# Performance work log

Measured on AMD Instinct MI355X. Metric: run time of the kernel, lower is better.

## Reference

```python
import jax, jax.numpy as jnp
import numpy as np

DIM = 512
HID = 2048
EPS = 1e-5


def setup_inputs() -> dict:
    key = jax.random.key(0)
    ks = jax.random.split(key, 11)
    B, S = 256, 100
    def lin(kw, fan_in, fan_out):
        # torch Linear init: U(-1/sqrt(fan_in), 1/sqrt(fan_in)); stored as [in, out]
        bound = 1.0 / np.sqrt(fan_in)
        return jax.random.uniform(kw, (fan_in, fan_out), jnp.float32, -bound, bound)
    def bias(kb, fan_in, fan_out):
        bound = 1.0 / np.sqrt(fan_in)
        return jax.random.uniform(kb, (fan_out,), jnp.float32, -bound, bound)
    return {
        "x": jax.random.normal(ks[0], (B, S, DIM), jnp.float32),
        "W_w": lin(ks[1], DIM, HID),  "W_b": bias(ks[2], DIM, HID),
        "WK_w": lin(ks[3], HID, HID), "WK_b": bias(ks[4], HID, HID),
        "WQ_w": lin(ks[5], HID, HID), "WQ_b": bias(ks[6], HID, HID),
        "WV_w": lin(ks[7], HID, HID), "WV_b": bias(ks[8], HID, HID),
        "W2_w": lin(ks[9], HID, DIM), "W2_b": bias(ks[10], HID, DIM),
    }


def reference(x, W_w, W_b, WK_w, WK_b, WQ_w, WQ_b, WV_w, WV_b, W2_w, W2_b):
    S = x.shape[1]
    # torch: tril(ones, diagonal=1) -> token i may attend to j <= i+1
    mask = jnp.tril(jnp.ones((S, S), dtype=bool), k=1)
    residual = x
    h = jax.nn.relu(x @ W_w + W_b)            # [B,S,HID]
    K = h @ WK_w + WK_b
    Q = h @ WQ_w + WQ_b
    V = h @ WV_w + WV_b
    # note: original scales by sqrt(dim)=sqrt(512), not sqrt(hidden_dim)
    attn = jnp.einsum('bqh,bkh->bqk', Q, K) / np.sqrt(DIM)
    attn = jnp.where(mask, attn, -jnp.inf)
    attn = jax.nn.softmax(attn, axis=-1)
    o = jnp.einsum('bqk,bkh->bqh', attn, V)
    y = o @ W2_w + W2_b + residual            # [B,S,DIM]
    # F.layer_norm over x.shape[1:] == (S, DIM), no affine
    mu = jnp.mean(y, axis=(1, 2), keepdims=True)
    var = jnp.var(y, axis=(1, 2), keepdims=True)
    return (y - mu) * jax.lax.rsqrt(var + EPS)
```

## Files before the change

### kernel.cpp

```cpp
#include <hip/hip_runtime.h>
#include <hip/hip_bf16.h>

typedef unsigned int u32;
typedef unsigned short u16;
typedef __attribute__((ext_vector_type(4))) float f32x4;
typedef __attribute__((ext_vector_type(8))) short s16x8;
typedef __attribute__((ext_vector_type(4))) u16 u16x4;
typedef __attribute__((ext_vector_type(8))) u16 u16x8;

#define DEVFN __device__ __forceinline__

DEVFN u16 f2bf(float f) {
  u32 x = __builtin_bit_cast(u32, f);
  u32 r = x + 0x7fffu + ((x >> 16) & 1u);
  return (u16)(r >> 16);
}

DEVFN float bf2f(u16 b) { return __builtin_bit_cast(float, (u32)b << 16); }

DEVFN void gload_lds16(const u16* g, u16* l) {
  __builtin_amdgcn_global_load_lds((const __attribute__((address_space(1))) u32*)g,
                                   (__attribute__((address_space(3))) u32*)l, 16, 0, 0);
}

#define KQV_PHASE(Q, VMWAIT, DOSTAGE)                                          \
  {                                                                            \
    if (DOSTAGE) {                                                             \
      const int g_ = (Q) + 2;                                                  \
      const int sl_ = (g_ & 3) * 8192;                                         \
      const int k0_ = (g_ >> 1) * 64 + (g_ & 1) * 32;                          \
      gload_lds16(aS0 + k0_, smemw + sl_ + ldst);                              \
      gload_lds16(aS1 + k0_, smemw + sl_ + 4096 + ldst);                       \
      gload_lds16(bS0 + k0_, smemw + 32768 + sl_ + ldst);                      \
      gload_lds16(bS1 + k0_, smemw + 32768 + sl_ + 4096 + ldst);               \
    }                                                                          \
    VMWAIT;                                                                    \
    __builtin_amdgcn_s_barrier();                                              \
    {                                                                          \
      const int sl_ = (Q) & 3;                                                 \
      const u16* As_ = smem + sl_ * 8192;                                      \
      const u16* Bs_ = smem + 32768 + sl_ * 8192;                              \
      s16x8 fa_[8], fb_[4];                                                    \
      _Pragma("unroll") for (int mf = 0; mf < 8; ++mf)                         \
          fa_[mf] = *(const s16x8*)(As_ + baseA + mf * 512);                   \
      _Pragma("unroll") for (int nf = 0; nf < 4; ++nf)                         \
          fb_[nf] = *(const s16x8*)(Bs_ + baseB + nf * 512);                   \
      __builtin_amdgcn_s_setprio(1);                                           \
      _Pragma("unroll") for (int mf = 0; mf < 8; ++mf)                         \
        _Pragma("unroll") for (int nf = 0; nf < 4; ++nf)                       \
          acc[mf][nf] = __builtin_amdgcn_mfma_f32_16x16x32_bf16(               \
              fa_[mf], fb_[nf], acc[mf][nf], 0, 0, 0);                         \
      __builtin_amdgcn_s_setprio(0);                                           \
    }                                                                          \
    __builtin_amdgcn_sched_barrier(0);                                         \
  }

#define WAITV4 asm volatile("s_waitcnt vmcnt(4)" ::: "memory")
#define WAITV0 asm volatile("s_waitcnt vmcnt(0)" ::: "memory")
#define WAITNONE ((void)0)

template<int RELU>
__launch_bounds__(512, 2)
__global__ void gemm256(const u16* __restrict__ Ag, int lda,
                        const u16* __restrict__ Bg, int ldb,
                        u16* __restrict__ C, int ldc,
                        const float* __restrict__ bias,
                        int M, int K, int ntiles) {
  extern __shared__ u16 smem_dyn[];
  const u16* smem = smem_dyn;
  u16* smemw = smem_dyn;

  const int tid = threadIdx.x;
  const int lane = tid & 63, wave = tid >> 6;
  const int wm = wave >> 2, wn = wave & 3;
  const int l15 = lane & 15, l4 = lane >> 4;

  const int nwg = gridDim.x;
  const int q8 = nwg >> 3, r8 = nwg & 7;
  const int xcd = blockIdx.x & 7, io = blockIdx.x >> 3;
  const int wg = (xcd < r8) ? (xcd * (q8 + 1) + io)
                            : (r8 * (q8 + 1) + (xcd - r8) * q8 + io);
  const int m0 = (wg / ntiles) * 256, n0 = (wg % ntiles) * 256;

  const int chunkSwz = (l4 ^ ((l15 >> 1) & 3)) * 8;
  const int baseA = (wm * 128 + l15) * 32 + chunkSwz;
  const int baseB = (wn * 64 + l15) * 32 + chunkSwz;

  const int srow = tid >> 2;
  const int scol = (((tid & 3) ^ ((tid >> 3) & 3))) * 8;
  long ar0 = m0 + srow;        if (ar0 > M - 1) ar0 = M - 1;
  long ar1 = m0 + 128 + srow;  if (ar1 > M - 1) ar1 = M - 1;
  const u16* aS0 = Ag + ar0 * (long)lda + scol;
  const u16* aS1 = Ag + ar1 * (long)lda + scol;
  const u16* bS0 = Bg + (long)(n0 + srow) * ldb + scol;
  const u16* bS1 = Bg + (long)(n0 + 128 + srow) * ldb + scol;
  const int ldst = tid * 8;

  f32x4 acc[8][4];
#pragma unroll
  for (int i = 0; i < 8; ++i)
#pragma unroll
    for (int j = 0; j < 4; ++j) acc[i][j] = (f32x4){0.f, 0.f, 0.f, 0.f};

  const int NT = K >> 6;

  {
#pragma unroll
    for (int g_ = 0; g_ < 2; ++g_) {
      const int k0_ = g_ * 32;
      gload_lds16(aS0 + k0_, smemw + g_ * 8192 + ldst);
      gload_lds16(aS1 + k0_, smemw + g_ * 8192 + 4096 + ldst);
      gload_lds16(bS0 + k0_, smemw + 32768 + g_ * 8192 + ldst);
      gload_lds16(bS1 + k0_, smemw + 32768 + g_ * 8192 + 4096 + ldst);
    }
    __builtin_amdgcn_sched_barrier(0);
  }

  for (int t = 0; t < NT - 1; ++t) {
    KQV_PHASE(2 * t,     WAITV4, true);
    KQV_PHASE(2 * t + 1, WAITV4, true);
  }
  KQV_PHASE(2 * NT - 2, WAITV0,   false);
  KQV_PHASE(2 * NT - 1, WAITNONE, false);

#pragma unroll
  for (int mf = 0; mf < 8; ++mf) {
#pragma unroll
    for (int nf = 0; nf < 4; ++nf) {
      const int n = n0 + wn * 64 + nf * 16 + l15;
      const float bv = bias[n];
#pragma unroll
      for (int r = 0; r < 4; ++r) {
        const int s = wm * 128 + mf * 16 + l4 * 4 + r;
        if (m0 + s >= M) continue;
        float v = acc[mf][nf][r] + bv;
        if (RELU) v = v > 0.f ? v : 0.f;
        C[(long)(m0 + s) * ldc + n] = f2bf(v);
      }
    }
  }
}

template<int MODE>
__launch_bounds__(256)
__global__ void gemm_bt(const u16* __restrict__ Ag, int lda, int aRPB, int aRowMax,
                        const u16* __restrict__ Bg, int ldb, int bRPB, int bRowMax,
                        void* __restrict__ Cptr, int ldc, int cRPB, int cRowGuard,
                        const float* __restrict__ bias, const float* __restrict__ resid,
                        int K, float scale, float* __restrict__ part, int pbase,
                        long sliceE) {
  __shared__ __align__(16) u16 As[128 * 64];
  __shared__ __align__(16) u16 Bs[128 * 64];
  const int tid = threadIdx.x;
  const int lane = tid & 63, wid = tid >> 6;
  const int l15 = lane & 15, l4 = lane >> 4;
  const int wr = wid >> 1, wc = wid & 1;
  const int m0 = blockIdx.x * 128, n0 = blockIdx.y * 128;
  int b = blockIdx.z;
  int zslice = 0;
  long koff = 0;
  if (MODE == 6) { zslice = b & 3; koff = (long)zslice * K; b >>= 2; }

  const u16* aSrc[4];
  const u16* bSrc[4];
  u16* aDst[4];
  u16* bDst[4];
#pragma unroll
  for (int i = 0; i < 4; ++i) {
    int c = i * 256 + tid;
    int r = c >> 3, g = c & 7;
    long arow = (long)b * aRPB + m0 + r; if (arow > aRowMax) arow = aRowMax;
    aSrc[i] = Ag + arow * (long)lda + koff + g * 8;
    aDst[i] = &As[c * 8];
    long brow = (long)b * bRPB + n0 + r; if (brow > bRowMax) brow = bRowMax;
    bSrc[i] = Bg + brow * (long)ldb + koff + g * 8;
    bDst[i] = &Bs[c * 8];
  }

  f32x4 acc[4][4];
#pragma unroll
  for (int i = 0; i < 4; ++i)
#pragma unroll
    for (int j = 0; j < 4; ++j) acc[i][j] = (f32x4){0.f, 0.f, 0.f, 0.f};

  for (int kt = 0; kt < K; kt += 64) {
#pragma unroll
    for (int i = 0; i < 4; ++i) gload_lds16(aSrc[i] + kt, aDst[i]);
#pragma unroll
    for (int i = 0; i < 4; ++i) gload_lds16(bSrc[i] + kt, bDst[i]);
    __syncthreads();
#pragma unroll
    for (int kk = 0; kk < 2; ++kk) {
      s16x8 af[4], bfr[4];
#pragma unroll
      for (int mi = 0; mi < 4; ++mi) {
        int rr = wr * 64 + mi * 16 + l15;
        af[mi] = *(const s16x8*)&As[rr * 64 + kk * 32 + l4 * 8];
      }
#pragma unroll
      for (int ni = 0; ni < 4; ++ni) {
        int rr = wc * 64 + ni * 16 + l15;
        bfr[ni] = *(const s16x8*)&Bs[rr * 64 + kk * 32 + l4 * 8];
      }
#pragma unroll
      for (int mi = 0; mi < 4; ++mi)
#pragma unroll
        for (int ni = 0; ni < 4; ++ni)
          acc[mi][ni] = __builtin_amdgcn_mfma_f32_16x16x32_bf16(af[mi], bfr[ni], acc[mi][ni], 0, 0, 0);
    }
    __syncthreads();
  }

  const long cRow0 = (long)b * cRPB + m0;
  float lsum = 0.f, lsq = 0.f;
#pragma unroll
  for (int mi = 0; mi < 4; ++mi) {
#pragma unroll
    for (int ni = 0; ni < 4; ++ni) {
      const int n = n0 + wc * 64 + ni * 16 + l15;
      float bv = 0.f;
      if (MODE == 4) bv = bias[n];
#pragma unroll
      for (int r = 0; r < 4; ++r) {
        const int s = wr * 64 + mi * 16 + l4 * 4 + r;
        if (m0 + s < cRowGuard) {
          const long ci = (cRow0 + s) * (long)ldc + n;
          float v = acc[mi][ni][r];
          if (MODE == 3)      { ((u16*)Cptr)[ci] = f2bf(v); }
          else if (MODE == 6) { ((float*)Cptr)[(long)zslice * sliceE + ci] = v * scale; }
          else                { v += bv + resid[ci]; ((float*)Cptr)[ci] = v;
                                lsum += v; lsq += v * v; }
        }
      }
    }
  }

  if (MODE == 4) {
    float* shs = (float*)As;
    float* shq = (float*)Bs;
    shs[tid] = lsum; shq[tid] = lsq;
    __syncthreads();
    for (int off = 128; off; off >>= 1) {
      if (tid < off) { shs[tid] += shs[tid + off]; shq[tid] += shq[tid + off]; }
      __syncthreads();
    }
    if (tid == 0) {
      part[((long)pbase + b) * 8 + blockIdx.y * 2]     = shs[0];
      part[((long)pbase + b) * 8 + blockIdx.y * 2 + 1] = shq[0];
    }
  }
}

__launch_bounds__(256)
__global__ void softmax_rows(const float* __restrict__ S, u16* __restrict__ P,
                             long sliceE) {
  const int wid = threadIdx.x >> 6, lane = threadIdx.x & 63;
  const long rowg = (long)blockIdx.x * 4 + wid;
  const int i = (int)(rowg & 127);
  const float* srow = S + rowg * 128;
  u16* prow = P + rowg * 128;
  if (i >= 100) { prow[lane] = 0; prow[lane + 64] = 0; return; }
  const int jmax = (i + 1 < 99) ? i + 1 : 99;
  bool v0 = lane <= jmax, v1 = (lane + 64) <= jmax;
  float a0 = srow[lane]            + srow[sliceE + lane] +
             srow[2 * sliceE + lane] + srow[3 * sliceE + lane];
  float a1 = srow[lane + 64]            + srow[sliceE + lane + 64] +
             srow[2 * sliceE + lane + 64] + srow[3 * sliceE + lane + 64];
  float s0 = v0 ? a0 : -3e38f;
  float s1 = v1 ? a1 : -3e38f;
  float m = fmaxf(s0, s1);
#pragma unroll
  for (int off = 32; off; off >>= 1) m = fmaxf(m, __shfl_xor(m, off));
  float e0 = v0 ? __expf(s0 - m) : 0.f;
  float e1 = v1 ? __expf(s1 - m) : 0.f;
  float sum = e0 + e1;
#pragma unroll
  for (int off = 32; off; off >>= 1) sum += __shfl_xor(sum, off);
  float rs = 1.f / sum;
  prow[lane] = f2bf(e0 * rs);
  prow[lane + 64] = f2bf(e1 * rs);
}

__launch_bounds__(256)
__global__ void transpose_cast_w(const float* __restrict__ W, u16* __restrict__ Wt,
                                 int K, int N) {
  __shared__ __align__(16) float t[64][68];
  const int tid = threadIdx.x;
  const int n0 = blockIdx.x * 64, k0 = blockIdx.y * 64;
#pragma unroll
  for (int it = 0; it < 4; ++it) {
    int c = it * 256 + tid;
    int r = c >> 4, cc = (c & 15) * 4;
    f32x4 v = *(const f32x4*)&W[(long)(k0 + r) * N + n0 + cc];
    *(f32x4*)&t[r][cc] = v;
  }
  __syncthreads();
#pragma unroll
  for (int it = 0; it < 4; ++it) {
    int c = it * 256 + tid;
    int n = c >> 4, kk = (c & 15) * 4;
    u16x4 o;
#pragma unroll
    for (int j = 0; j < 4; ++j) o[j] = f2bf(t[kk + j][n]);
    *(u16x4*)&Wt[(long)(n0 + n) * K + k0 + kk] = o;
  }
}

__launch_bounds__(256)
__global__ void cast_f32_to_bf16(const float* __restrict__ in, u16* __restrict__ out, long n4) {
  for (long i = (long)blockIdx.x * 256 + threadIdx.x; i < n4; i += (long)gridDim.x * 256) {
    f32x4 v = *(const f32x4*)&in[i * 4];
    u16x4 o;
#pragma unroll
    for (int j = 0; j < 4; ++j) o[j] = f2bf(v[j]);
    *(u16x4*)&out[i * 4] = o;
  }
}

__launch_bounds__(256)
__global__ void rowdot_f32(const float* __restrict__ M, const float* __restrict__ v,
                           float* __restrict__ o, int ncols) {
  __shared__ float red[4];
  const float* r = M + (long)blockIdx.x * ncols;
  const int tid = threadIdx.x;
  float s = 0.f;
  for (int d = tid; d < ncols; d += 256) s += r[d] * v[d];
#pragma unroll
  for (int off = 32; off; off >>= 1) s += __shfl_down(s, off);
  if ((tid & 63) == 0) red[tid >> 6] = s;
  __syncthreads();
  if (tid == 0) o[blockIdx.x] = red[0] + red[1] + red[2] + red[3];
}

__launch_bounds__(256)
__global__ void bias_w2(const float* __restrict__ bV, const float* __restrict__ W2w,
                        float* __restrict__ o) {
  int n = blockIdx.x * 256 + threadIdx.x;
  float s = 0.f;
  for (int h = 0; h < 2048; ++h) s += bV[h] * W2w[h * 512 + n];
  o[n] = s;
}

__launch_bounds__(256)
__global__ void transpose_vt(const u16* __restrict__ V, u16* __restrict__ Vt,
                             int vstride, int nH) {
  __shared__ __align__(16) u16 t[64][72];
  const int tid = threadIdx.x;
  const int h0 = blockIdx.x * 64, s0 = blockIdx.y * 64, b = blockIdx.z;
#pragma unroll
  for (int it = 0; it < 2; ++it) {
    int c = it * 256 + tid;
    int s = c >> 3, hh = (c & 7) * 8;
    u16x8 v = {0, 0, 0, 0, 0, 0, 0, 0};
    if (s0 + s < 100) v = *(const u16x8*)&V[((long)b * 100 + s0 + s) * vstride + h0 + hh];
    *(u16x8*)&t[s][hh] = v;
  }
  __syncthreads();
#pragma unroll
  for (int it = 0; it < 2; ++it) {
    int c = it * 256 + tid;
    int h = c >> 3, ss = (c & 7) * 8;
    u16x8 o;
#pragma unroll
    for (int j = 0; j < 8; ++j) o[j] = t[ss + j][h];
    *(u16x8*)&Vt[((long)b * nH + h0 + h) * 128 + s0 + ss] = o;
  }
}

__launch_bounds__(256)
__global__ void ln_apply(float* __restrict__ y, const float* __restrict__ part) {
  const long i4 = (long)blockIdx.x * 256 + threadIdx.x;
  const int b = (int)(i4 / 12800);
  const float* pb = part + (long)b * 8;
  const float s = pb[0] + pb[2] + pb[4] + pb[6];
  const float q = pb[1] + pb[3] + pb[5] + pb[7];
  const float mean = s * (1.f / 51200.f);
  const float var = q * (1.f / 51200.f) - mean * mean;
  const float rstd = rsqrtf(var + 1e-5f);
  f32x4 v = *(const f32x4*)&y[i4 * 4];
#pragma unroll
  for (int j = 0; j < 4; ++j) v[j] = (v[j] - mean) * rstd;
  *(f32x4*)&y[i4 * 4] = v;
}

extern "C" void kernel_launch(void* const* d_in, const int* in_sizes, int n_in,
                              void* d_out, int out_size, void* d_ws, size_t ws_size,
                              hipStream_t stream) {
  const float* x    = (const float*)d_in[0];
  const float* W_w  = (const float*)d_in[1];
  const float* W_b  = (const float*)d_in[2];
  const float* WK_w = (const float*)d_in[3];
  const float* WK_b = (const float*)d_in[4];
  const float* WQ_w = (const float*)d_in[5];
  const float* WQ_b = (const float*)d_in[6];
  const float* WV_w = (const float*)d_in[7];
  const float* WV_b = (const float*)d_in[8];
  const float* W2_w = (const float*)d_in[9];
  const float* W2_b = (const float*)d_in[10];
  float* out = (float*)d_out;
  const float SC = 0.044194173824159216f;

  const size_t FIXED = 26214400ull + 2097152ull + 10485760ull + 2097152ull +
                       10240ull + 8192ull + 262144ull;
  const size_t PERB = 1347584ull;
  const size_t PREPOVL = 25165824ull + 65536ull;
  int CH = 256;
  if (ws_size == 0) CH = 32;
  else {
    while (CH > 4) {
      size_t chunkBytes = (size_t)CH * PERB;
      if (chunkBytes < PREPOVL) chunkBytes = PREPOVL;
      if (FIXED + chunkBytes + 4096 <= ws_size) break;
      CH >>= 1;
    }
  }
  const int NCH = 256 / CH;
  const int CHR = CH * 100;
  const int MT256 = (CHR + 255) / 256;
  const long SLICE = (long)CH * 16384;

  char* p = (char*)d_ws;
  auto carve = [&](size_t bytes) { char* r = p; p += (bytes + 255) & ~(size_t)255; return r; };
  u16* xb     = (u16*)carve(26214400);
  u16* W1t    = (u16*)carve(2097152);
  u16* WTt    = (u16*)carve(10485760);
  u16* W2t    = (u16*)carve(2097152);
  float* bias2 = (float*)carve(10240);
  float* part = (float*)carve(8192);
  char* chunk0 = p;
  u16* h    = (u16*)carve((size_t)CH * 409600);
  u16* TW   = (u16*)carve((size_t)CH * 512000);
  float* sc = (float*)carve((size_t)CH * 262144);
  u16* P    = (u16*)carve((size_t)CH * 32768);
  u16* VW2T = (u16*)carve((size_t)CH * 131072);
  u16* WVb = (u16*)chunk0;
  u16* WKb = WVb + 2048 * 2048;
  u16* WQb = WKb + 2048 * 2048;

  cast_f32_to_bf16<<<2048, 256, 0, stream>>>(x, xb, 3276800);
  cast_f32_to_bf16<<<1024, 256, 0, stream>>>(WV_w, WVb, 1048576);
  cast_f32_to_bf16<<<1024, 256, 0, stream>>>(WK_w, WKb, 1048576);
  cast_f32_to_bf16<<<1024, 256, 0, stream>>>(WQ_w, WQb, 1048576);
  transpose_cast_w<<<dim3(32, 8), 256, 0, stream>>>(W_w,  W1t, 512, 2048);
  transpose_cast_w<<<dim3(8, 32), 256, 0, stream>>>(W2_w, W2t, 2048, 512);
  gemm_bt<3><<<dim3(16, 16, 1), 256, 0, stream>>>(WKb, 2048, 0, 2047, WQb, 2048, 0, 2047,
                                                  WTt, 2048, 0, 1 << 30,
                                                  nullptr, nullptr, 2048, 1.f,
                                                  nullptr, 0, 0);
  gemm_bt<3><<<dim3(4, 16, 1), 256, 0, stream>>>(W2t, 2048, 0, 511, WVb, 2048, 0, 2047,
                                                 WTt + (size_t)2048 * 2048, 2048, 0, 1 << 30,
                                                 nullptr, nullptr, 2048, 1.f,
                                                 nullptr, 0, 0);
  rowdot_f32<<<2048, 256, 0, stream>>>(WK_w, WQ_b, bias2, 2048);
  bias_w2<<<2, 256, 0, stream>>>(WV_b, W2_w, bias2 + 2048);

  for (int c = 0; c < NCH; ++c) {
    const u16* xc = xb + (size_t)c * CHR * 512;
    const float* xf = x + (size_t)c * CHR * 512;
    float* outc = out + (size_t)c * CHR * 512;

    gemm256<1><<<MT256 * 8, 512, 131072, stream>>>(xc, 512, W1t, 512,
                                                   h, 2048, W_b, CHR, 512, 8);
    gemm256<0><<<MT256 * 10, 512, 131072, stream>>>(h, 2048, WTt, 2048,
                                                    TW, 2560, bias2, CHR, 2048, 10);
    gemm_bt<6><<<dim3(1, 1, CH * 4), 256, 0, stream>>>(TW, 2560, 100, CHR - 1,
                                                       h, 2048, 100, CHR - 1,
                                                       sc, 128, 128, 1 << 30, nullptr, nullptr,
                                                       512, SC, nullptr, 0, SLICE);
    softmax_rows<<<CH * 32, 256, 0, stream>>>(sc, P, SLICE);
    transpose_vt<<<dim3(8, 2, CH), 256, 0, stream>>>(TW + 2048, VW2T, 2560, 512);
    gemm_bt<4><<<dim3(1, 4, CH), 256, 0, stream>>>(P, 128, 128, CH * 128 - 1,
                                                   VW2T, 128, 512, CH * 512 - 1,
                                                   outc, 512, 100, 100, W2_b, xf, 128, 1.f,
                                                   part, c * CH, 0);
  }

  ln_apply<<<12800, 256, 0, stream>>>(out, part);
}
```

Baseline: 795.8 us.

## Fuse score GEMM, softmax and PV/output GEMM into one attention kernel

Replaces the split-K score GEMM, the separate softmax kernel and the P·(VW2) GEMM with a single fused_attn kernel per batch and half of the query rows. Scores stay in LDS, softmax runs there, and the output GEMM plus residual and layer-norm partial sums happen in the same block. This removes the fp32 score buffer and P round trips and several launches, and also merges the three weight casts into one launch. In exchange each batch gets only 2 blocks with a full K=2048 loop and no split-K, which lowers parallelism, and LDS use per block grows.

```diff
diff --git a/kernel.cpp b/kernel.cpp
--- a/kernel.cpp
+++ b/kernel.cpp
@@ -147,8 +147,7 @@
                         const u16* __restrict__ Bg, int ldb, int bRPB, int bRowMax,
                         void* __restrict__ Cptr, int ldc, int cRPB, int cRowGuard,
                         const float* __restrict__ bias, const float* __restrict__ resid,
-                        int K, float scale, float* __restrict__ part, int pbase,
-                        long sliceE) {
+                        int K, float scale) {
   __shared__ __align__(16) u16 As[128 * 64];
   __shared__ __align__(16) u16 Bs[128 * 64];
   const int tid = threadIdx.x;
@@ -156,10 +155,7 @@
   const int l15 = lane & 15, l4 = lane >> 4;
   const int wr = wid >> 1, wc = wid & 1;
   const int m0 = blockIdx.x * 128, n0 = blockIdx.y * 128;
-  int b = blockIdx.z;
-  int zslice = 0;
-  long koff = 0;
-  if (MODE == 6) { zslice = b & 3; koff = (long)zslice * K; b >>= 2; }
+  const int b = blockIdx.z;
 
   const u16* aSrc[4];
   const u16* bSrc[4];
@@ -170,10 +166,10 @@
     int c = i * 256 + tid;
     int r = c >> 3, g = c & 7;
     long arow = (long)b * aRPB + m0 + r; if (arow > aRowMax) arow = aRowMax;
-    aSrc[i] = Ag + arow * (long)lda + koff + g * 8;
+    aSrc[i] = Ag + arow * (long)lda + g * 8;
     aDst[i] = &As[c * 8];
     long brow = (long)b * bRPB + n0 + r; if (brow > bRowMax) brow = bRowMax;
-    bSrc[i] = Bg + brow * (long)ldb + koff + g * 8;
+    bSrc[i] = Bg + brow * (long)ldb + g * 8;
     bDst[i] = &Bs[c * 8];
   }
 
@@ -212,73 +208,186 @@
   }
 
   const long cRow0 = (long)b * cRPB + m0;
-  float lsum = 0.f, lsq = 0.f;
 #pragma unroll
   for (int mi = 0; mi < 4; ++mi) {
 #pragma unroll
     for (int ni = 0; ni < 4; ++ni) {
       const int n = n0 + wc * 64 + ni * 16 + l15;
-      float bv = 0.f;
-      if (MODE == 4) bv = bias[n];
 #pragma unroll
       for (int r = 0; r < 4; ++r) {
         const int s = wr * 64 + mi * 16 + l4 * 4 + r;
         if (m0 + s < cRowGuard) {
           const long ci = (cRow0 + s) * (long)ldc + n;
-          float v = acc[mi][ni][r];
-          if (MODE == 3)      { ((u16*)Cptr)[ci] = f2bf(v); }
-          else if (MODE == 6) { ((float*)Cptr)[(long)zslice * sliceE + ci] = v * scale; }
-          else                { v += bv + resid[ci]; ((float*)Cptr)[ci] = v;
-                                lsum += v; lsq += v * v; }
+          ((u16*)Cptr)[ci] = f2bf(acc[mi][ni][r]);
         }
       }
     }
   }
-
-  if (MODE == 4) {
-    float* shs = (float*)As;
-    float* shq = (float*)Bs;
-    shs[tid] = lsum; shq[tid] = lsq;
+}
+
+__launch_bounds__(256)
+__global__ void fused_attn(const u16* __restrict__ TWc, const u16* __restrict__ hc,
+                           const u16* __restrict__ VW2T, const float* __restrict__ b2,
+                           const float* __restrict__ xf, float* __restrict__ outc,
+                           float* __restrict__ part, int pbase, float SC) {
+  __shared__ __align__(16) u16 As[64 * 64];
+  __shared__ __align__(16) u16 Bs[128 * 64];
+  __shared__ __align__(16) float Ss[64][132];
+  __shared__ __align__(16) u16 Ps[64][136];
+  const int tid = threadIdx.x;
+  const int lane = tid & 63, wave = tid >> 6;
+  const int l15 = lane & 15, l4 = lane >> 4;
+  const int wr = wave >> 1, wc = wave & 1;
+  const int rh = blockIdx.x;
+  const int b = blockIdx.z;
+
+  const u16* aSrc[2]; u16* aDst[2];
+  const u16* bSrc[4]; u16* bDst[4];
+#pragma unroll
+  for (int i = 0; i < 2; ++i) {
+    int c = i * 256 + tid, r = c >> 3, g = c & 7;
+    int ar = rh * 64 + r; if (ar > 99) ar = 99;
+    aSrc[i] = TWc + ((long)b * 100 + ar) * 2560 + g * 8;
+    aDst[i] = &As[c * 8];
+  }
+#pragma unroll
+  for (int i = 0; i < 4; ++i) {
+    int c = i * 256 + tid, r = c >> 3, g = c & 7;
+    int br = r > 99 ? 99 : r;
+    bSrc[i] = hc + ((long)b * 100 + br) * 2048 + g * 8;
+    bDst[i] = &Bs[c * 8];
+  }
+  f32x4 acc[2][4];
+#pragma unroll
+  for (int i = 0; i < 2; ++i)
+#pragma unroll
+    for (int j = 0; j < 4; ++j) acc[i][j] = (f32x4){0.f, 0.f, 0.f, 0.f};
+
+  for (int kt = 0; kt < 2048; kt += 64) {
+#pragma unroll
+    for (int i = 0; i < 2; ++i) gload_lds16(aSrc[i] + kt, aDst[i]);
+#pragma unroll
+    for (int i = 0; i < 4; ++i) gload_lds16(bSrc[i] + kt, bDst[i]);
     __syncthreads();
-    for (int off = 128; off; off >>= 1) {
-      if (tid < off) { shs[tid] += shs[tid + off]; shq[tid] += shq[tid + off]; }
+#pragma unroll
+    for (int kk = 0; kk < 2; ++kk) {
+      s16x8 af[2], bfr[4];
+#pragma unroll
+      for (int mi = 0; mi < 2; ++mi) {
+        int rr = wr * 32 + mi * 16 + l15;
+        af[mi] = *(const s16x8*)&As[rr * 64 + kk * 32 + l4 * 8];
+      }
+#pragma unroll
+      for (int ni = 0; ni < 4; ++ni) {
+        int rr = wc * 64 + ni * 16 + l15;
+        bfr[ni] = *(const s16x8*)&Bs[rr * 64 + kk * 32 + l4 * 8];
+      }
+#pragma unroll
+      for (int mi = 0; mi < 2; ++mi)
+#pragma unroll
+        for (int ni = 0; ni < 4; ++ni)
+          acc[mi][ni] = __builtin_amdgcn_mfma_f32_16x16x32_bf16(af[mi], bfr[ni], acc[mi][ni], 0, 0, 0);
+    }
+    __syncthreads();
+  }
+#pragma unroll
+  for (int mi = 0; mi < 2; ++mi)
+#pragma unroll
+    for (int ni = 0; ni < 4; ++ni)
+#pragma unroll
+      for (int r = 0; r < 4; ++r)
+        Ss[wr * 32 + mi * 16 + l4 * 4 + r][wc * 64 + ni * 16 + l15] = acc[mi][ni][r] * SC;
+  __syncthreads();
+
+  for (int rr = wave * 16; rr < wave * 16 + 16; ++rr) {
+    const int qi = rh * 64 + rr;
+    if (qi >= 100) { Ps[rr][lane] = 0; Ps[rr][lane + 64] = 0; continue; }
+    const int jmax = (qi + 1 < 99) ? qi + 1 : 99;
+    bool v0 = lane <= jmax, v1 = lane + 64 <= jmax;
+    float s0 = v0 ? Ss[rr][lane] : -3e38f;
+    float s1 = v1 ? Ss[rr][lane + 64] : -3e38f;
+    float m = fmaxf(s0, s1);
+#pragma unroll
+    for (int off = 32; off; off >>= 1) m = fmaxf(m, __shfl_xor(m, off));
+    float e0 = v0 ? __expf(s0 - m) : 0.f;
+    float e1 = v1 ? __expf(s1 - m) : 0.f;
+    float sum = e0 + e1;
+#pragma unroll
+    for (int off = 32; off; off >>= 1) sum += __shfl_xor(sum, off);
+    float rs = 1.f / sum;
+    Ps[rr][lane] = f2bf(e0 * rs);
+    Ps[rr][lane + 64] = f2bf(e1 * rs);
+  }
+  __syncthreads();
+
+  float lsum = 0.f, lsq = 0.f;
+  for (int nt = 0; nt < 4; ++nt) {
+    f32x4 a2[2][4];
+#pragma unroll
+    for (int i = 0; i < 2; ++i)
+#pragma unroll
+      for (int j = 0; j < 4; ++j) a2[i][j] = (f32x4){0.f, 0.f, 0.f, 0.f};
+    for (int kt2 = 0; kt2 < 2; ++kt2) {
       __syncthreads();
-    }
-    if (tid == 0) {
-      part[((long)pbase + b) * 8 + blockIdx.y * 2]     = shs[0];
-      part[((long)pbase + b) * 8 + blockIdx.y * 2 + 1] = shq[0];
-    }
-  }
-}
-
-__launch_bounds__(256)
-__global__ void softmax_rows(const float* __restrict__ S, u16* __restrict__ P,
-                             long sliceE) {
-  const int wid = threadIdx.x >> 6, lane = threadIdx.x & 63;
-  const long rowg = (long)blockIdx.x * 4 + wid;
-  const int i = (int)(rowg & 127);
-  const float* srow = S + rowg * 128;
-  u16* prow = P + rowg * 128;
-  if (i >= 100) { prow[lane] = 0; prow[lane + 64] = 0; return; }
-  const int jmax = (i + 1 < 99) ? i + 1 : 99;
-  bool v0 = lane <= jmax, v1 = (lane + 64) <= jmax;
-  float a0 = srow[lane]            + srow[sliceE + lane] +
-             srow[2 * sliceE + lane] + srow[3 * sliceE + lane];
-  float a1 = srow[lane + 64]            + srow[sliceE + lane + 64] +
-             srow[2 * sliceE + lane + 64] + srow[3 * sliceE + lane + 64];
-  float s0 = v0 ? a0 : -3e38f;
-  float s1 = v1 ? a1 : -3e38f;
-  float m = fmaxf(s0, s1);
-#pragma unroll
-  for (int off = 32; off; off >>= 1) m = fmaxf(m, __shfl_xor(m, off));
-  float e0 = v0 ? __expf(s0 - m) : 0.f;
-  float e1 = v1 ? __expf(s1 - m) : 0.f;
-  float sum = e0 + e1;
-#pragma unroll
-  for (int off = 32; off; off >>= 1) sum += __shfl_xor(sum, off);
-  float rs = 1.f / sum;
-  prow[lane] = f2bf(e0 * rs);
-  prow[lane + 64] = f2bf(e1 * rs);
+#pragma unroll
+      for (int i = 0; i < 4; ++i) {
+        int c = i * 256 + tid, r = c >> 3, g = c & 7;
+        gload_lds16(VW2T + ((long)b * 512 + nt * 128 + r) * 128 + kt2 * 64 + g * 8, &Bs[c * 8]);
+      }
+      __syncthreads();
+#pragma unroll
+      for (int kk = 0; kk < 2; ++kk) {
+        s16x8 af2[2], bf2[4];
+#pragma unroll
+        for (int mi = 0; mi < 2; ++mi) {
+          int rr = wr * 32 + mi * 16 + l15;
+          af2[mi] = *(const s16x8*)&Ps[rr][kt2 * 64 + kk * 32 + l4 * 8];
+        }
+#pragma unroll
+        for (int ni = 0; ni < 4; ++ni) {
+          int rr = wc * 64 + ni * 16 + l15;
+          bf2[ni] = *(const s16x8*)&Bs[rr * 64 + kk * 32 + l4 * 8];
+        }
+#pragma unroll
+        for (int mi = 0; mi < 2; ++mi)
+#pragma unroll
+          for (int ni = 0; ni < 4; ++ni)
+            a2[mi][ni] = __builtin_amdgcn_mfma_f32_16x16x32_bf16(af2[mi], bf2[ni], a2[mi][ni], 0, 0, 0);
+      }
+    }
+#pragma unroll
+    for (int mi = 0; mi < 2; ++mi) {
+#pragma unroll
+      for (int ni = 0; ni < 4; ++ni) {
+        const int n = nt * 128 + wc * 64 + ni * 16 + l15;
+        const float bv = b2[n];
+#pragma unroll
+        for (int r = 0; r < 4; ++r) {
+          const int s = wr * 32 + mi * 16 + l4 * 4 + r;
+          const int qi = rh * 64 + s;
+          if (qi < 100) {
+            const long ci = ((long)b * 100 + qi) * 512 + n;
+            float v = a2[mi][ni][r] + bv + xf[ci];
+            outc[ci] = v;
+            lsum += v; lsq += v * v;
+          }
+        }
+      }
+    }
+  }
+  __syncthreads();
+  float* shs = (float*)Ss;
+  float* shq = shs + 256;
+  shs[tid] = lsum; shq[tid] = lsq;
+  __syncthreads();
+  for (int off = 128; off; off >>= 1) {
+    if (tid < off) { shs[tid] += shs[tid + off]; shq[tid] += shq[tid + off]; }
+    __syncthreads();
+  }
+  if (tid == 0) {
+    part[((long)pbase + b) * 8 + rh * 2]     = shs[0];
+    part[((long)pbase + b) * 8 + rh * 2 + 1] = shq[0];
+  }
 }
 
 __launch_bounds__(256)
@@ -315,6 +424,21 @@
     for (int j = 0; j < 4; ++j) o[j] = f2bf(v[j]);
     *(u16x4*)&out[i * 4] = o;
   }
+}
+
+__launch_bounds__(256)
+__global__ void cast3_w(const float* __restrict__ a, const float* __restrict__ b,
+                        const float* __restrict__ c, u16* __restrict__ oa,
+                        u16* __restrict__ ob, u16* __restrict__ oc) {
+  const int seg = blockIdx.x >> 12;
+  const long i = ((long)(blockIdx.x & 4095) * 256 + threadIdx.x);
+  const float* in = seg == 0 ? a : (seg == 1 ? b : c);
+  u16* out = seg == 0 ? oa : (seg == 1 ? ob : oc);
+  f32x4 v = *(const f32x4*)&in[i * 4];
+  u16x4 o;
+#pragma unroll
+  for (int j = 0; j < 4; ++j) o[j] = f2bf(v[j]);
+  *(u16x4*)&out[i * 4] = o;
 }
 
 __launch_bounds__(256)
@@ -372,8 +496,8 @@
   const long i4 = (long)blockIdx.x * 256 + threadIdx.x;
   const int b = (int)(i4 / 12800);
   const float* pb = part + (long)b * 8;
-  const float s = pb[0] + pb[2] + pb[4] + pb[6];
-  const float q = pb[1] + pb[3] + pb[5] + pb[7];
+  const float s = pb[0] + pb[2];
+  const float q = pb[1] + pb[3];
   const float mean = s * (1.f / 51200.f);
   const float var = q * (1.f / 51200.f) - mean * mean;
   const float rstd = rsqrtf(var + 1e-5f);
@@ -402,7 +526,7 @@
 
   const size_t FIXED = 26214400ull + 2097152ull + 10485760ull + 2097152ull +
                        10240ull + 8192ull + 262144ull;
-  const size_t PERB = 1347584ull;
+  const size_t PERB = 1052672ull;
   const size_t PREPOVL = 25165824ull + 65536ull;
   int CH = 256;
   if (ws_size == 0) CH = 32;
@@ -417,7 +541,6 @@
   const int NCH = 256 / CH;
   const int CHR = CH * 100;
   const int MT256 = (CHR + 255) / 256;
-  const long SLICE = (long)CH * 16384;
 
   char* p = (char*)d_ws;
   auto carve = [&](size_t bytes) { char* r = p; p += (bytes + 255) & ~(size_t)255; return r; };
@@ -430,27 +553,21 @@
   char* chunk0 = p;
   u16* h    = (u16*)carve((size_t)CH * 409600);
   u16* TW   = (u16*)carve((size_t)CH * 512000);
-  float* sc = (float*)carve((size_t)CH * 262144);
-  u16* P    = (u16*)carve((size_t)CH * 32768);
   u16* VW2T = (u16*)carve((size_t)CH * 131072);
   u16* WVb = (u16*)chunk0;
   u16* WKb = WVb + 2048 * 2048;
   u16* WQb = WKb + 2048 * 2048;
 
   cast_f32_to_bf16<<<2048, 256, 0, stream>>>(x, xb, 3276800);
-  cast_f32_to_bf16<<<1024, 256, 0, stream>>>(WV_w, WVb, 1048576);
-  cast_f32_to_bf16<<<1024, 256, 0, stream>>>(WK_w, WKb, 1048576);
-  cast_f32_to_bf16<<<1024, 256, 0, stream>>>(WQ_w, WQb, 1048576);
+  cast3_w<<<12288, 256, 0, stream>>>(WV_w, WK_w, WQ_w, WVb, WKb, WQb);
   transpose_cast_w<<<dim3(32, 8), 256, 0, stream>>>(W_w,  W1t, 512, 2048);
   transpose_cast_w<<<dim3(8, 32), 256, 0, stream>>>(W2_w, W2t, 2048, 512);
   gemm_bt<3><<<dim3(16, 16, 1), 256, 0, stream>>>(WKb, 2048, 0, 2047, WQb, 2048, 0, 2047,
                                                   WTt, 2048, 0, 1 << 30,
-                                                  nullptr, nullptr, 2048, 1.f,
-                                                  nullptr, 0, 0);
+                                                  nullptr, nullptr, 2048, 1.f);
   gemm_bt<3><<<dim3(4, 16, 1), 256, 0, stream>>>(W2t, 2048, 0, 511, WVb, 2048, 0, 2047,
                                                  WTt + (size_t)2048 * 2048, 2048, 0, 1 << 30,
-                                                 nullptr, nullptr, 2048, 1.f,
-                                                 nullptr, 0, 0);
+                                                 nullptr, nullptr, 2048, 1.f);
   rowdot_f32<<<2048, 256, 0, stream>>>(WK_w, WQ_b, bias2, 2048);
   bias_w2<<<2, 256, 0, stream>>>(WV_b, W2_w, bias2 + 2048);
 
@@ -463,16 +580,9 @@
                                                    h, 2048, W_b, CHR, 512, 8);
     gemm256<0><<<MT256 * 10, 512, 131072, stream>>>(h, 2048, WTt, 2048,
                                                     TW, 2560, bias2, CHR, 2048, 10);
-    gemm_bt<6><<<dim3(1, 1, CH * 4), 256, 0, stream>>>(TW, 2560, 100, CHR - 1,
-                                                       h, 2048, 100, CHR - 1,
-                                                       sc, 128, 128, 1 << 30, nullptr, nullptr,
-                                                       512, SC, nullptr, 0, SLICE);
-    softmax_rows<<<CH * 32, 256, 0, stream>>>(sc, P, SLICE);
     transpose_vt<<<dim3(8, 2, CH), 256, 0, stream>>>(TW + 2048, VW2T, 2560, 512);
-    gemm_bt<4><<<dim3(1, 4, CH), 256, 0, stream>>>(P, 128, 128, CH * 128 - 1,
-                                                   VW2T, 128, 512, CH * 512 - 1,
-                                                   outc, 512, 100, 100, W2_b, xf, 128, 1.f,
-                                                   part, c * CH, 0);
+    fused_attn<<<dim3(2, 1, CH), 256, 0, stream>>>(TW, h, VW2T, W2_b, xf, outc,
+                                                   part, c * CH, SC);
   }
 
   ln_apply<<<12800, 256, 0, stream>>>(out, part);
```

New measurement: 841.2 us. 5.7% more time.

## Fuse V transpose into the KQV GEMM epilogue and merge weight casts

Applied to the files above, without the earlier changes.

The projection GEMM now writes its V-side output tiles straight into the per-batch transposed layout that the attention-times-V GEMM consumes. This drops the separate transpose_vt kernel and the extra TW columns it read from, which also shrinks the per-chunk workspace. The three weight-cast launches are merged into a single kernel. The transposed epilogue stores are strided 2-byte writes with poor coalescing. The padding rows 100..127 of VW2T are no longer zeroed, which could let uninitialised data leak into results.

```diff
diff --git a/kernel.cpp b/kernel.cpp
--- a/kernel.cpp
+++ b/kernel.cpp
@@ -59,11 +59,12 @@
 #define WAITV0 asm volatile("s_waitcnt vmcnt(0)" ::: "memory")
 #define WAITNONE ((void)0)
 
-template<int RELU>
+template<int RELU, int SPLIT>
 __launch_bounds__(512, 2)
 __global__ void gemm256(const u16* __restrict__ Ag, int lda,
                         const u16* __restrict__ Bg, int ldb,
                         u16* __restrict__ C, int ldc,
+                        u16* __restrict__ C2,
                         const float* __restrict__ bias,
                         int M, int K, int ntiles) {
   extern __shared__ u16 smem_dyn[];
@@ -135,7 +136,13 @@
         if (m0 + s >= M) continue;
         float v = acc[mf][nf][r] + bv;
         if (RELU) v = v > 0.f ? v : 0.f;
-        C[(long)(m0 + s) * ldc + n] = f2bf(v);
+        if (SPLIT && n0 >= 2048) {
+          const int m = m0 + s;
+          const int b = m / 100, si = m - b * 100;
+          C2[((long)b * 512 + (n - 2048)) * 128 + si] = f2bf(v);
+        } else {
+          C[(long)(m0 + s) * ldc + n] = f2bf(v);
+        }
       }
     }
   }
@@ -318,6 +325,21 @@
 }
 
 __launch_bounds__(256)
+__global__ void cast3_w(const float* __restrict__ a, const float* __restrict__ b,
+                        const float* __restrict__ c, u16* __restrict__ oa,
+                        u16* __restrict__ ob, u16* __restrict__ oc) {
+  const int seg = blockIdx.x >> 12;
+  const long i = ((long)(blockIdx.x & 4095) * 256 + threadIdx.x);
+  const float* in = seg == 0 ? a : (seg == 1 ? b : c);
+  u16* out = seg == 0 ? oa : (seg == 1 ? ob : oc);
+  f32x4 v = *(const f32x4*)&in[i * 4];
+  u16x4 o;
+#pragma unroll
+  for (int j = 0; j < 4; ++j) o[j] = f2bf(v[j]);
+  *(u16x4*)&out[i * 4] = o;
+}
+
+__launch_bounds__(256)
 __global__ void rowdot_f32(const float* __restrict__ M, const float* __restrict__ v,
                            float* __restrict__ o, int ncols) {
   __shared__ float red[4];
@@ -339,32 +361,6 @@
   float s = 0.f;
   for (int h = 0; h < 2048; ++h) s += bV[h] * W2w[h * 512 + n];
   o[n] = s;
-}
-
-__launch_bounds__(256)
-__global__ void transpose_vt(const u16* __restrict__ V, u16* __restrict__ Vt,
-                             int vstride, int nH) {
-  __shared__ __align__(16) u16 t[64][72];
-  const int tid = threadIdx.x;
-  const int h0 = blockIdx.x * 64, s0 = blockIdx.y * 64, b = blockIdx.z;
-#pragma unroll
-  for (int it = 0; it < 2; ++it) {
-    int c = it * 256 + tid;
-    int s = c >> 3, hh = (c & 7) * 8;
-    u16x8 v = {0, 0, 0, 0, 0, 0, 0, 0};
-    if (s0 + s < 100) v = *(const u16x8*)&V[((long)b * 100 + s0 + s) * vstride + h0 + hh];
-    *(u16x8*)&t[s][hh] = v;
-  }
-  __syncthreads();
-#pragma unroll
-  for (int it = 0; it < 2; ++it) {
-    int c = it * 256 + tid;
-    int h = c >> 3, ss = (c & 7) * 8;
-    u16x8 o;
-#pragma unroll
-    for (int j = 0; j < 8; ++j) o[j] = t[ss + j][h];
-    *(u16x8*)&Vt[((long)b * nH + h0 + h) * 128 + s0 + ss] = o;
-  }
 }
 
 __launch_bounds__(256)
@@ -402,7 +398,7 @@
 
   const size_t FIXED = 26214400ull + 2097152ull + 10485760ull + 2097152ull +
                        10240ull + 8192ull + 262144ull;
-  const size_t PERB = 1347584ull;
+  const size_t PERB = 1245184ull;
   const size_t PREPOVL = 25165824ull + 65536ull;
   int CH = 256;
   if (ws_size == 0) CH = 32;
@@ -429,7 +425,7 @@
   float* part = (float*)carve(8192);
   char* chunk0 = p;
   u16* h    = (u16*)carve((size_t)CH * 409600);
-  u16* TW   = (u16*)carve((size_t)CH * 512000);
+  u16* TW   = (u16*)carve((size_t)CH * 409600);
   float* sc = (float*)carve((size_t)CH * 262144);
   u16* P    = (u16*)carve((size_t)CH * 32768);
   u16* VW2T = (u16*)carve((size_t)CH * 131072);
@@ -438,9 +434,7 @@
   u16* WQb = WKb + 2048 * 2048;
 
   cast_f32_to_bf16<<<2048, 256, 0, stream>>>(x, xb, 3276800);
-  cast_f32_to_bf16<<<1024, 256, 0, stream>>>(WV_w, WVb, 1048576);
-  cast_f32_to_bf16<<<1024, 256, 0, stream>>>(WK_w, WKb, 1048576);
-  cast_f32_to_bf16<<<1024, 256, 0, stream>>>(WQ_w, WQb, 1048576);
+  cast3_w<<<12288, 256, 0, stream>>>(WV_w, WK_w, WQ_w, WVb, WKb, WQb);
   transpose_cast_w<<<dim3(32, 8), 256, 0, stream>>>(W_w,  W1t, 512, 2048);
   transpose_cast_w<<<dim3(8, 32), 256, 0, stream>>>(W2_w, W2t, 2048, 512);
   gemm_bt<3><<<dim3(16, 16, 1), 256, 0, stream>>>(WKb, 2048, 0, 2047, WQb, 2048, 0, 2047,
@@ -459,16 +453,15 @@
     const float* xf = x + (size_t)c * CHR * 512;
     float* outc = out + (size_t)c * CHR * 512;
 
-    gemm256<1><<<MT256 * 8, 512, 131072, stream>>>(xc, 512, W1t, 512,
-                                                   h, 2048, W_b, CHR, 512, 8);
-    gemm256<0><<<MT256 * 10, 512, 131072, stream>>>(h, 2048, WTt, 2048,
-                                                    TW, 2560, bias2, CHR, 2048, 10);
-    gemm_bt<6><<<dim3(1, 1, CH * 4), 256, 0, stream>>>(TW, 2560, 100, CHR - 1,
+    gemm256<1, 0><<<MT256 * 8, 512, 131072, stream>>>(xc, 512, W1t, 512,
+                                                      h, 2048, nullptr, W_b, CHR, 512, 8);
+    gemm256<0, 1><<<MT256 * 10, 512, 131072, stream>>>(h, 2048, WTt, 2048,
+                                                       TW, 2048, VW2T, bias2, CHR, 2048, 10);
+    gemm_bt<6><<<dim3(1, 1, CH * 4), 256, 0, stream>>>(TW, 2048, 100, CHR - 1,
                                                        h, 2048, 100, CHR - 1,
                                                        sc, 128, 128, 1 << 30, nullptr, nullptr,
                                                        512, SC, nullptr, 0, SLICE);
     softmax_rows<<<CH * 32, 256, 0, stream>>>(sc, P, SLICE);
-    transpose_vt<<<dim3(8, 2, CH), 256, 0, stream>>>(TW + 2048, VW2T, 2560, 512);
     gemm_bt<4><<<dim3(1, 4, CH), 256, 0, stream>>>(P, 128, 128, CH * 128 - 1,
                                                    VW2T, 128, 512, CH * 512 - 1,
                                                    outc, 512, 100, 100, W2_b, xf, 128, 1.f,
```

Measured after the change: 901.4 us. +13.3%, slower.
